# Kernel tuning notes

Hardware: AMD Instinct MI355X
Metric: run time of the kernel (lower is better)

Reference implementation:

```python
import jax, jax.numpy as jnp
import numpy as np

B, DIM, OC, H, W, HEADS = 4, 128, 128, 128, 128, 8
L = H * W
_BN_INV = 1.0 / (1.0 + 1e-5) ** 0.5  # eval-mode BN: running_mean=0, running_var=1


def conv2d(x, w, b=None, groups=1, pad=0):
    y = jax.lax.conv_general_dilated(
        x, w, (1, 1), [(pad, pad), (pad, pad)],
        dimension_numbers=('NCHW', 'OIHW', 'NCHW'),
        feature_group_count=groups)
    if b is not None:
        y = y + b[None, :, None, None]
    return y


def bn(x, g, b):
    return x * (g * _BN_INV)[None, :, None, None] + b[None, :, None, None]


def ln(x, g, b, eps=1e-5):
    m = jnp.mean(x, -1, keepdims=True)
    v = jnp.mean((x - m) ** 2, -1, keepdims=True)
    return (x - m) * jax.lax.rsqrt(v + eps) * g + b


def rope_tables(h, w, c, base=10000.0):
    k_max = c // 4
    theta = 1.0 / base ** (np.arange(k_max, dtype=np.float32) / k_max)
    gi, gj = np.meshgrid(np.arange(h, dtype=np.float32),
                         np.arange(w, dtype=np.float32), indexing='ij')
    ang = np.concatenate([gi[..., None] * theta, gj[..., None] * theta], -1)  # (h,w,c//2)
    return jnp.asarray(np.cos(ang)), jnp.asarray(np.sin(ang))


def apply_rope(x, cs, sn):  # x: (b,h,w,c); consecutive pairs = (re, im)
    xr, xi = x[..., 0::2], x[..., 1::2]
    return jnp.stack([cs * xr - sn * xi, sn * xr + cs * xi], -1).reshape(x.shape)


def linear_attn(x, qk_w, qk_b, lepe_w, lepe_b, h, w):
    b, n, c = x.shape
    hd = c // HEADS
    qk = x @ qk_w.T + qk_b
    q = jax.nn.elu(qk[..., :c]) + 1.0
    k = jax.nn.elu(qk[..., c:]) + 1.0
    cs, sn = rope_tables(h, w, c)

    def heads(t):  # (b,n,c) -> (b,HEADS,n,hd)
        return t.reshape(b, n, HEADS, hd).transpose(0, 2, 1, 3)

    q_r = heads(apply_rope(q.reshape(b, h, w, c), cs, sn).reshape(b, n, c))
    k_r = heads(apply_rope(k.reshape(b, h, w, c), cs, sn).reshape(b, n, c))
    qh, kh, vh = heads(q), heads(k), heads(x)
    k_mean = jnp.mean(kh, axis=2, keepdims=True)                      # (b,Hd,1,hd)
    z = 1.0 / (jnp.einsum('bhnd,bhmd->bhnm', qh, k_mean) + 1e-6)      # (b,Hd,n,1)
    s = n ** -0.5
    kv = jnp.einsum('bhnd,bhne->bhde', k_r * s, vh * s)               # (b,Hd,hd,hd)
    out = jnp.einsum('bhnd,bhde->bhne', q_r, kv) * z
    out = out.transpose(0, 2, 1, 3).reshape(b, n, c)
    v_img = x.reshape(b, h, w, c).transpose(0, 3, 1, 2)
    lepe = conv2d(v_img, lepe_w, lepe_b, groups=c, pad=1)
    return out + lepe.transpose(0, 2, 3, 1).reshape(b, n, c)


def fmt_block(xb, fw1, fb1, f_g, f_be, fw2, fb2, n_g, n_be):
    t = jnp.fft.fft2(xb)                                              # (B,C,H,W) complex
    wgt = jax.nn.relu(bn(conv2d(t.real, fw1, fb1), f_g, f_be))
    wgt = jax.nn.sigmoid(conv2d(wgt, fw2, fb2))
    f = jnp.abs(jnp.fft.ifft2(wgt * t))
    f = jax.nn.relu(bn(f, n_g, n_be))
    return f.reshape(f.shape[0], f.shape[1], -1).transpose(0, 2, 1)   # (B,L,C)


def _forward(x, c1_w, c1_b, c1_g, c1_be, cpe1_w, cpe1_b,
             fw1, fb1, f_g, f_be, fw2, fb2, nbn_g, nbn_be,
             ln1_g, ln1_b, d3w1, d3b1, d3w2, d5w1, d5b1, d5w2,
             ap_w, ap_b, ip2_w, ip2_b, dwc2_w, dwc2_b,
             qk_w, qk_b, lepe_w, lepe_b, op_w, op_b,
             cpe2_w, cpe2_b, ln2_g, ln2_b,
             ffn_w1, ffn_b1, ffn_w2, ffn_b2, po_w,
             red_w, red_b, red_g, red_be):
    Bb, C, Hh, Ww = x.shape
    Ll = Hh * Ww
    to_img = lambda t: t.reshape(Bb, Hh, Ww, C).transpose(0, 3, 1, 2)   # (B,L,C)->(B,C,H,W)
    to_seq = lambda t: t.transpose(0, 2, 3, 1).reshape(Bb, Ll, -1)       # (B,C,H,W)->(B,L,C)

    x_0 = jax.nn.relu(bn(conv2d(x, c1_w, c1_b), c1_g, c1_be))           # (B,OC,H,W)
    xt = to_seq(x + conv2d(x, cpe1_w, cpe1_b, groups=C, pad=1))
    shortcut = xt
    fmt1 = fmt_block(to_img(xt), fw1, fb1, f_g, f_be, fw2, fb2, nbn_g, nbn_be)

    x_s = ln(xt, ln1_g, ln1_b)
    xs_img = to_img(x_s)
    x_s3 = conv2d(conv2d(xs_img, d3w1, d3b1), d3w2, None, groups=C // 2, pad=1)
    x_s5 = conv2d(conv2d(xs_img, d5w1, d5b1), d5w2, None, groups=C // 2, pad=2)
    act_res = jax.nn.silu(to_seq(conv2d(xs_img, ap_w, ap_b)))

    def branch(t):  # (B,C/2,H,W) -> (B,L,C/2)
        t = conv2d(t, ip2_w, ip2_b)
        t = jax.nn.silu(conv2d(t, dwc2_w, dwc2_b, groups=C // 2, pad=1))
        return to_seq(t)

    a3 = linear_attn(branch(x_s3), qk_w, qk_b, lepe_w, lepe_b, Hh, Ww)
    a5 = linear_attn(branch(x_s5), qk_w, qk_b, lepe_w, lepe_b, Hh, Ww)
    xs = jnp.concatenate([a3, a5], -1)
    xs = to_seq(conv2d(to_img(xs * act_res), op_w, op_b))

    xt = shortcut + xs + fmt1
    xt = xt + to_seq(conv2d(to_img(xt), cpe2_w, cpe2_b, groups=C, pad=1))
    fmt2 = fmt_block(to_img(xt), fw1, fb1, f_g, f_be, fw2, fb2, nbn_g, nbn_be)
    h2 = ln(xt, ln2_g, ln2_b)
    ffn = jax.nn.gelu(h2 @ ffn_w1.T + ffn_b1, approximate=False) @ ffn_w2.T + ffn_b2
    xt = xt + ffn + fmt2

    xo = conv2d(to_img(xt), po_w)                                        # (B,OC,H,W)
    cat = jnp.concatenate([x_0, xo], 1)
    return jax.nn.relu(bn(conv2d(cat, red_w, red_b), red_g, red_be)) + x_0


def setup_inputs():
    key = jax.random.key(0)
    it = iter(jax.random.split(key, 64))

    def w(shape, s=0.05):
        return jax.random.normal(next(it), shape, jnp.float32) * s

    d, oc = DIM, OC
    ones = lambda n: jnp.ones((n,), jnp.float32)
    zeros = lambda n: jnp.zeros((n,), jnp.float32)
    return {
        'x': jax.random.normal(next(it), (B, d, H, W), jnp.float32),
        'c1_w': w((oc, d, 1, 1)), 'c1_b': w((oc,), 0.01), 'c1_g': ones(oc), 'c1_be': zeros(oc),
        'cpe1_w': w((d, 1, 3, 3)), 'cpe1_b': w((d,), 0.01),
        'fw1': w((d // 16, d, 1, 1)), 'fb1': w((d // 16,), 0.01),
        'f_g': ones(d // 16), 'f_be': zeros(d // 16),
        'fw2': w((d, d // 16, 1, 1)), 'fb2': w((d,), 0.01),
        'nbn_g': ones(d), 'nbn_be': zeros(d),
        'ln1_g': ones(d), 'ln1_b': zeros(d),
        'd3w1': w((d, d, 1, 1)), 'd3b1': w((d,), 0.01), 'd3w2': w((d // 2, 2, 3, 3)),
        'd5w1': w((d, d, 1, 1)), 'd5b1': w((d,), 0.01), 'd5w2': w((d // 2, 2, 5, 5)),
        'ap_w': w((d, d, 1, 1)), 'ap_b': w((d,), 0.01),
        'ip2_w': w((d // 2, d // 2, 1, 1)), 'ip2_b': w((d // 2,), 0.01),
        'dwc2_w': w((d // 2, 1, 3, 3)), 'dwc2_b': w((d // 2,), 0.01),
        'qk_w': w((d, d // 2)), 'qk_b': w((d,), 0.01),
        'lepe_w': w((d // 2, 1, 3, 3)), 'lepe_b': w((d // 2,), 0.01),
        'op_w': w((d, d, 1, 1)), 'op_b': w((d,), 0.01),
        'cpe2_w': w((d, 1, 3, 3)), 'cpe2_b': w((d,), 0.01),
        'ln2_g': ones(d), 'ln2_b': zeros(d),
        'ffn_w1': w((4, d)), 'ffn_b1': w((4,), 0.01),
        'ffn_w2': w((d, 4)), 'ffn_b2': w((d,), 0.01),
        'po_w': w((oc, d, 1, 1)),
        'red_w': w((oc, 2 * oc, 1, 1)), 'red_b': w((oc,), 0.01),
        'red_g': ones(oc), 'red_be': zeros(oc),
    }


def reference(x, c1_w, c1_b, c1_g, c1_be, cpe1_w, cpe1_b,
              fw1, fb1, f_g, f_be, fw2, fb2, nbn_g, nbn_be,
              ln1_g, ln1_b, d3w1, d3b1, d3w2, d5w1, d5b1, d5w2,
              ap_w, ap_b, ip2_w, ip2_b, dwc2_w, dwc2_b,
              qk_w, qk_b, lepe_w, lepe_b, op_w, op_b,
              cpe2_w, cpe2_b, ln2_g, ln2_b,
              ffn_w1, ffn_b1, ffn_w2, ffn_b2, po_w,
              red_w, red_b, red_g, red_be):
    return _forward(x, c1_w, c1_b, c1_g, c1_be, cpe1_w, cpe1_b,
                    fw1, fb1, f_g, f_be, fw2, fb2, nbn_g, nbn_be,
                    ln1_g, ln1_b, d3w1, d3b1, d3w2, d5w1, d5b1, d5w2,
                    ap_w, ap_b, ip2_w, ip2_b, dwc2_w, dwc2_b,
                    qk_w, qk_b, lepe_w, lepe_b, op_w, op_b,
                    cpe2_w, cpe2_b, ln2_g, ln2_b,
                    ffn_w1, ffn_b1, ffn_w2, ffn_b2, po_w,
                    red_w, red_b, red_g, red_be)
```

## Files before the change

kernel.cpp:

```cpp
#include <hip/hip_runtime.h>
#include <math.h>

typedef unsigned short bf16_t;
typedef __attribute__((ext_vector_type(8))) short short8;
typedef __attribute__((ext_vector_type(4))) float f32x4;

#define B_ 4
#define C_ 128
#define H_ 128
#define W_ 128
#define L_ (H_*W_)
#define NS  ((size_t)B_*L_*C_)
#define NH  ((size_t)B_*L_*64)
#define NSP ((size_t)L_*C_)
#define PI_F 3.14159265358979323846f
#define BN_INV 0.9999950000374997f
#define THETA_SC 0.8304820237218406f
#define TOTW 157148
#define W16SHIFT 107548
#define WOFF_PO 107612
#define WOFF_RED 123996

#define W2_ 66
#define L2_ (128*W2_)
// ... 230 lines not shown
  }
}

__global__ __launch_bounds__(256) void k_fft_col_inv_scaled_h(
    bf16_t* __restrict__ re, bf16_t* __restrict__ im,
    const float* __restrict__ wg1, const float* __restrict__ fw2,
    const float* __restrict__ fb2) {
  __shared__ float Lre[128][34];
  __shared__ float Lim[128][34];
  __shared__ float w2r[8];
  int tid = threadIdx.x;
  size_t img = blockIdx.x >> 1;
  int c = (int)(img & 127);
  int b = (int)(img >> 7);
  int w0 = (blockIdx.x & 1) * 33;
  if (tid < 8) w2r[tid] = fw2[c*8 + tid];
  float b2 = fb2[c];
  bf16_t* rp = re + img * (size_t)L2_ + w0;
  bf16_t* ip = im + img * (size_t)L2_ + w0;
  const float* wgp = wg1 + (size_t)b*8*L2_ + w0;
  __syncthreads();
  for (int i = tid; i < 4224; i += 256) {
    int h = i / 33, wl = i - h*33;
    size_t p = (size_t)h*W2_ + wl;
    float a = b2;
    #pragma unroll
    for (int o = 0; o < 8; o++) a += w2r[o] * wgp[(size_t)o*L2_ + p];
    float wgt = 1.f/(1.f+expf(-a));
    Lre[h][wl] = ldf(rp[p]) * wgt;
    Lim[h][wl] = ldf(ip[p]) * wgt;
  }
  __syncthreads();
  int lane = tid & 63, wv = tid >> 6;
  float tc[7], ts[7];
  tw_inv(lane, tc, ts);
  for (int col = wv; col < 33; col += 4) {
    float lor = Lre[lane][col], loi = Lim[lane][col];
    float hir = Lre[lane+64][col], hii = Lim[lane+64][col];
    fft128_inv(lor, loi, hir, hii, lane, tc, ts);
    Lre[lane][col]=lor*(1.f/128.f); Lim[lane][col]=loi*(1.f/128.f);
    Lre[lane+64][col]=hir*(1.f/128.f); Lim[lane+64][col]=hii*(1.f/128.f);
  }
  __syncthreads();
  for (int i = tid; i < 4224; i += 256) {
    int h = i / 33, wl = i - h*33;
    rp[(size_t)h*W2_ + wl] = f2b(Lre[h][wl]);
    ip[(size_t)h*W2_ + wl] = f2b(Lim[h][wl]);
  }
}

__global__ __launch_bounds__(256) void k_fft_row_inv_abs_seq_h(
    const bf16_t* __restrict__ re, const bf16_t* __restrict__ im,
    const float* __restrict__ ng, const float* __restrict__ nbe,
    const float* __restrict__ add1, const float* __restrict__ add2,
    float* __restrict__ out) {
  __shared__ float S[64*132];
  int tid = threadIdx.x;
  int bid = blockIdx.x;
  int ch = (bid & 1) * 64;
  int h  = (bid >> 1) & 127;
  int b  = bid >> 8;
  {
    const bf16_t* rbase = re + (size_t)(b*128 + ch)*L2_ + (size_t)h*W2_;
    const bf16_t* ibase = im + (size_t)(b*128 + ch)*L2_ + (size_t)h*W2_;
    for (int i = tid; i < 64*66; i += 256) {
      int c = i / 66, v = i - c*66;
      S[c*132 + v]      = ldf(rbase[(size_t)c*L2_ + v]);
      S[c*132 + 66 + v] = ldf(ibase[(size_t)c*L2_ + v]);
    }
  }
  __syncthreads();
  int lane = tid & 63, wv = tid >> 6;
  int rb = (int)(__brev((unsigned)lane) >> 26);
  int vlo = 2*rb, vhi = vlo + 1;
  float tc[7], ts[7];
  tw_inv(lane, tc, ts);
  float rr[8][4];
  #pragma unroll
  for (int t = 0; t < 8; t++) {
    int ca = wv*16 + 2*t, cb = ca + 1;
    const float* Sa = S + ca*132;
    const float* Sb = S + cb*132;
    float lor, loi, hir, hii;
    if (vlo <= 64) {
      float ar = Sa[vlo], ai = Sa[66+vlo], br = Sb[vlo], bi = Sb[66+vlo];
      lor = ar - bi; loi = ai + br;
    } else {
      int u = 128 - vlo;
      float ar = Sa[u], ai = Sa[66+u], br = Sb[u], bi = Sb[66+u];
      lor = ar + bi; loi = br - ai;
    }
    if (vhi <= 64) {
      float ar = Sa[vhi], ai = Sa[66+vhi], br = Sb[vhi], bi = Sb[66+vhi];
      hir = ar - bi; hii = ai + br;
    } else {
      int u = 128 - vhi;
      float ar = Sa[u], ai = Sa[66+u], br = Sb[u], bi = Sb[66+u];
      hir = ar + bi; hii = br - ai;
    }
    fft128_inv(lor, loi, hir, hii, lane, tc, ts);
    rr[t][0] = fabsf(lor);
    rr[t][1] = fabsf(loi);
    rr[t][2] = fabsf(hir);
    rr[t][3] = fabsf(hii);
  }
  __syncthreads();
  float* T = S;
  #pragma unroll
  for (int t = 0; t < 8; t++) {
    int ca = wv*16 + 2*t, cb = ca + 1;
    float sga = ng[ch+ca]*BN_INV, sba = nbe[ch+ca];
    float sgb = ng[ch+cb]*BN_INV, sbb = nbe[ch+cb];
    T[ca*130 + lane]      = fmaxf(rr[t][0]*(1.f/128.f)*sga + sba, 0.f);
    T[cb*130 + lane]      = fmaxf(rr[t][1]*(1.f/128.f)*sgb + sbb, 0.f);
    T[ca*130 + 64 + lane] = fmaxf(rr[t][2]*(1.f/128.f)*sga + sba, 0.f);
    T[cb*130 + 64 + lane] = fmaxf(rr[t][3]*(1.f/128.f)*sgb + sbb, 0.f);
  }
  __syncthreads();
  size_t sb0 = ((size_t)b*L_ + (size_t)h*128)*128 + ch;
  #pragma unroll
  for (int it = 0; it < 8; it++) {
    int idx = it*256 + tid;
    int c4 = (idx & 15)*4, w = idx >> 4;
    size_t off = sb0 + (size_t)w*128 + c4;
    float4 v;
    v.x = T[(c4+0)*130 + w];
    v.y = T[(c4+1)*130 + w];
    v.z = T[(c4+2)*130 + w];
    v.w = T[(c4+3)*130 + w];
    float4 x1 = *(const float4*)(add1 + off);
    float4 x2 = *(const float4*)(add2 + off);
    v.x += x1.x + x2.x; v.y += x1.y + x2.y;
    v.z += x1.z + x2.z; v.w += x1.w + x2.w;
    *(float4*)(out + off) = v;
  }
}

__global__ __launch_bounds__(256) void k_freq1_h(const bf16_t* __restrict__ tre,
    const float* __restrict__ fw1, const float* __restrict__ fb1,
    const float* __restrict__ fg, const float* __restrict__ fbe,
    float* __restrict__ wg1) {
  __shared__ float w1s[1024];
  int tid = threadIdx.x;
  for (int i = tid; i < 1024; i += 256) w1s[i] = fw1[i];
  __syncthreads();
  size_t g = (size_t)blockIdx.x*256 + tid;
  int p = (int)(g % L2_);
  int b = (int)(g / L2_);
  const bf16_t* tp = tre + (size_t)b*128*L2_ + p;
  float acc[8];
  #pragma unroll
  for (int o = 0; o < 8; o++) acc[o] = 0.f;
  for (int c = 0; c < 128; c++) {
    float v = ldf(tp[(size_t)c*L2_]);
    #pragma unroll
    for (int o = 0; o < 8; o++) acc[o] += w1s[o*128+c]*v;
  }
  size_t ob = (size_t)b*8*L2_ + p;
  #pragma unroll
  for (int o = 0; o < 8; o++) {
    float v = (acc[o] + fb1[o]) * (fg[o]*BN_INV) + fbe[o];
    wg1[ob + (size_t)o*L2_] = fmaxf(v, 0.f);
  }
}

template<bool DUAL>
__global__ void k_p2s(const void* __restrict__ src, float* __restrict__ dst,
                      const float* __restrict__ add1, const float* __restrict__ add2,
                      const int* __restrict__ flagp) {
  __shared__ float tile[32][33];
  int fl = DUAL ? *flagp : 1;
  int b = blockIdx.z;
  int p0 = blockIdx.x*32, c0 = blockIdx.y*32;
  int tx = threadIdx.x, ty = threadIdx.y;
  size_t base_in = (size_t)b*NSP;
  #pragma unroll
  for (int k = 0; k < 4; k++) {
    size_t off = base_in + (size_t)(c0+ty+8*k)*L_ + p0 + tx;
    float v;
    if (DUAL && !fl) v = ldf(((const bf16_t*)src)[off]);
    else             v = ((const float*)src)[off];
    tile[ty+8*k][tx] = v;
  }
  __syncthreads();
  size_t base = (size_t)b*NSP;
  #pragma unroll
  for (int k = 0; k < 4; k++) {
    size_t idx = base + (size_t)(p0+ty+8*k)*C_ + c0 + tx;
    float v = tile[tx][ty+8*k];
    if (add1) v += add1[idx];
    if (add2) v += add2[idx];
    dst[idx] = v;
  }
}

template<int CC>
__global__ __launch_bounds__(256) void k_dw3(const float* __restrict__ in,
    const float* __restrict__ w, const float* __restrict__ bias,
    float* __restrict__ out) {
  __shared__ float wl[9*CC];
  int tid = threadIdx.x;
  for (int i = tid; i < 9*CC; i += 256) {
    int tap = i / CC, ch = i % CC;
    wl[i] = w[ch*9 + tap];
  }
  __syncthreads();
  size_t g = (size_t)blockIdx.x*256 + tid;
  int c = (int)(g & (CC-1));
  float wr[9];
  #pragma unroll
  for (int t = 0; t < 9; t++) wr[t] = wl[t*CC + c];
  size_t s = g / CC;
  int w0 = (int)(s & 31) * 4;
  int hp = (int)((s >> 5) & 127);
  int b  = (int)(s >> 12);
  const float* ip = in + (size_t)b*L_*CC + c;
  float bi = bias[c];
  float a0 = bi, a1 = bi, a2 = bi, a3 = bi;
  #pragma unroll
  for (int dh = -1; dh <= 1; dh++) {
    int h2 = hp + dh;
    if ((unsigned)h2 >= 128u) continue;
    const float* rp = ip + (size_t)h2*W_*CC;
    float px[6];
    #pragma unroll
    for (int x = 0; x < 6; x++) {
      int w2 = w0 - 1 + x;
      px[x] = ((unsigned)w2 < 128u) ? rp[(size_t)w2*CC] : 0.f;
    }
    #pragma unroll
    for (int dw = 0; dw < 3; dw++) {
      float f = wr[(dh+1)*3 + dw];
      a0 += f*px[dw];   a1 += f*px[dw+1];
      a2 += f*px[dw+2]; a3 += f*px[dw+3];
    }
  }
  size_t tb = (size_t)b*L_ + (size_t)hp*W_ + w0;
  out[(tb+0)*CC + c] = in[(tb+0)*CC + c] + a0;
  out[(tb+1)*CC + c] = in[(tb+1)*CC + c] + a1;
  out[(tb+2)*CC + c] = in[(tb+2)*CC + c] + a2;
  out[(tb+3)*CC + c] = in[(tb+3)*CC + c] + a3;
}

__global__ __launch_bounds__(256) void k_dw3h(const bf16_t* __restrict__ in,
    const float* __restrict__ w, const float* __restrict__ bias,
    bf16_t* __restrict__ out) {
  __shared__ float wl[9*64];
  int tid = threadIdx.x;
  for (int i = tid; i < 9*64; i += 256) {
    int tap = i / 64, ch = i % 64;
    wl[i] = w[ch*9 + tap];
  }
  __syncthreads();
  size_t g = (size_t)blockIdx.x*256 + tid;
  int c = (int)(g & 63);
  float wr[9];
  #pragma unroll
  for (int t = 0; t < 9; t++) wr[t] = wl[t*64 + c];
  size_t s = g >> 6;
  int w0 = (int)(s & 31) * 4;
  int hp = (int)((s >> 5) & 127);
  int b  = (int)(s >> 12);
  const bf16_t* ip = in + (size_t)b*L_*64 + c;
  float bi = bias[c];
  float a0 = bi, a1 = bi, a2 = bi, a3 = bi;
  #pragma unroll
  for (int dh = -1; dh <= 1; dh++) {
    int h2 = hp + dh;
    if ((unsigned)h2 >= 128u) continue;
    const bf16_t* rp = ip + (size_t)h2*W_*64;
    float px[6];
    #pragma unroll
    for (int x = 0; x < 6; x++) {
      int w2 = w0 - 1 + x;
      px[x] = ((unsigned)w2 < 128u) ? ldf(rp[(size_t)w2*64]) : 0.f;
    }
    #pragma unroll
    for (int dw = 0; dw < 3; dw++) {
      float f = wr[(dh+1)*3 + dw];
      a0 += f*px[dw];   a1 += f*px[dw+1];
      a2 += f*px[dw+2]; a3 += f*px[dw+3];
    }
  }
  size_t tb = (size_t)b*L_ + (size_t)hp*W_ + w0;
  out[(tb+0)*64 + c] = f2b(a0 / (1.f + expf(-a0)));
  out[(tb+1)*64 + c] = f2b(a1 / (1.f + expf(-a1)));
  out[(tb+2)*64 + c] = f2b(a2 / (1.f + expf(-a2)));
  out[(tb+3)*64 + c] = f2b(a3 / (1.f + expf(-a3)));
}

template<int K>
__global__ __launch_bounds__(256) void k_gconv(const bf16_t* __restrict__ in,
    const float* __restrict__ w, bf16_t* __restrict__ out) {
  __shared__ float wl[K*K*128];
// ... 16 lines not shown
  int hp = (int)((s >> 5) & 127);
  int b  = (int)(s >> 12);
  const bf16_t* ip = in + (size_t)b*L_*128 + 2*oc;
  constexpr int P = K/2;
  float a0 = 0.f, a1 = 0.f, a2 = 0.f, a3 = 0.f;
  #pragma unroll
  for (int kh = 0; kh < K; kh++) {
    int h2 = hp + kh - P;
    if ((unsigned)h2 >= 128u) continue;
    const bf16_t* rp = ip + (size_t)h2*W_*128;
    float2 px[K+3];
    #pragma unroll
    for (int x = 0; x < K+3; x++) {
      int w2 = w0 - P + x;
      if ((unsigned)w2 < 128u) {
        unsigned uv = *(const unsigned*)(rp + (size_t)w2*128);
        px[x] = make_float2(ldf((bf16_t)(uv & 0xffffu)), ldf((bf16_t)(uv >> 16)));
      } else px[x] = make_float2(0.f, 0.f);
    }
    #pragma unroll
    for (int kw = 0; kw < K; kw++) {
      float fx = wx[kh*K + kw], fy = wy[kh*K + kw];
      a0 += fx*px[kw+0].x + fy*px[kw+0].y;
      a1 += fx*px[kw+1].x + fy*px[kw+1].y;
      a2 += fx*px[kw+2].x + fy*px[kw+2].y;
      a3 += fx*px[kw+3].x + fy*px[kw+3].y;
    }
  }
  size_t tb = (size_t)b*L_ + (size_t)hp*W_ + w0;
  out[(tb+0)*64 + oc] = f2b(a0);
  out[(tb+1)*64 + oc] = f2b(a1);
  out[(tb+2)*64 + oc] = f2b(a2);
  out[(tb+3)*64 + oc] = f2b(a3);
}

template<int CIN, int COUT, int EPI, bool MUL, bool IB16, bool OB16>
__global__ __launch_bounds__(256) void k_mfma_tok(
    const void* __restrict__ in, const bf16_t* __restrict__ mulp,
    const bf16_t* __restrict__ W16, const float* __restrict__ bias,
    void* __restrict__ out) {
  constexpr int NO = COUT/16;
  constexpr int KS = (CIN >= 128) ? 4 : (CIN/32);
  int tid = threadIdx.x;
  int lane = tid & 63, wv = tid >> 6;
  int m = lane & 15, q = lane >> 4;
  size_t t0 = (size_t)blockIdx.x*64 + (size_t)wv*16;
  f32x4 acc[NO];
  #pragma unroll
  for (int i = 0; i < NO; i++) acc[i] = (f32x4){0.f,0.f,0.f,0.f};
  for (int kc = 0; kc < CIN; kc += KS*32) {
    short8 afv[KS];
    if (IB16) {
      #pragma unroll
      for (int kk = 0; kk < KS; kk++)
        afv[kk] = *(const short8*)((const bf16_t*)in + (t0 + m)*CIN + kc + kk*32 + q*8);
    } else {
      float4 A[KS][2];
      #pragma unroll
      for (int kk = 0; kk < KS; kk++) {
        const float* ap = (const float*)in + (t0 + m)*CIN + kc + kk*32 + q*8;
        A[kk][0] = *(const float4*)ap;
        A[kk][1] = *(const float4*)(ap + 4);
      }
      if (MUL) {
        #pragma unroll
        for (int kk = 0; kk < KS; kk++) {
          const bf16_t* mp = mulp + (t0 + m)*CIN + kc + kk*32 + q*8;
          union { bf16_t u[8]; short8 v; } mv;
          mv.v = *(const short8*)mp;
          A[kk][0].x*=ldf(mv.u[0]); A[kk][0].y*=ldf(mv.u[1]);
          A[kk][0].z*=ldf(mv.u[2]); A[kk][0].w*=ldf(mv.u[3]);
          A[kk][1].x*=ldf(mv.u[4]); A[kk][1].y*=ldf(mv.u[5]);
          A[kk][1].z*=ldf(mv.u[6]); A[kk][1].w*=ldf(mv.u[7]);
        }
      }
      #pragma unroll
      for (int kk = 0; kk < KS; kk++) {
        union { short s[8]; short8 v; } af;
        af.s[0]=(short)f2b(A[kk][0].x); af.s[1]=(short)f2b(A[kk][0].y);
        af.s[2]=(short)f2b(A[kk][0].z); af.s[3]=(short)f2b(A[kk][0].w);
        af.s[4]=(short)f2b(A[kk][1].x); af.s[5]=(short)f2b(A[kk][1].y);
        af.s[6]=(short)f2b(A[kk][1].z); af.s[7]=(short)f2b(A[kk][1].w);
        afv[kk] = af.v;
      }
    }
    #pragma unroll
    for (int kk = 0; kk < KS; kk++) {
      #pragma unroll
      for (int o = 0; o < NO; o++) {
        short8 bf = *(const short8*)(W16 + (size_t)(o*16 + m)*CIN + kc + kk*32 + q*8);
        acc[o] = __builtin_amdgcn_mfma_f32_16x16x32_bf16(afv[kk], bf, acc[o], 0, 0, 0);
      }
    }
  }
  #pragma unroll
  for (int o = 0; o < NO; o++) {
    float bv = (EPI >= 1) ? bias[o*16 + m] : 0.f;
    #pragma unroll
    for (int r = 0; r < 4; r++) {
      int row = q*4 + r;
      float v = acc[o][r] + bv;
      if (EPI == 2) v = v / (1.f + expf(-v));
      if (EPI == 3) v = v > 0.f ? v + 1.f : expf(v);
      size_t idx = (t0 + row)*COUT + o*16 + m;
      if (OB16) ((bf16_t*)out)[idx] = f2b(v);
      else      ((float*)out)[idx] = v;
    }
  }
}

__global__ __launch_bounds__(256) void k_mfma_ln3(
    const float* __restrict__ in,
    const float* __restrict__ lng, const float* __restrict__ lnb,
    const bf16_t* __restrict__ Wd3, const float* __restrict__ bd3,
    const bf16_t* __restrict__ Wd5, const float* __restrict__ bd5,
    const bf16_t* __restrict__ Wap, const float* __restrict__ bap,
    bf16_t* __restrict__ outd3, bf16_t* __restrict__ outd5, bf16_t* __restrict__ outap) {
  __shared__ float gs[128], bs[128];
  __shared__ bf16_t T16[64*130];
  int tid = threadIdx.x;
  if (tid < 128) { gs[tid] = lng[tid]; bs[tid] = lnb[tid]; }
  __syncthreads();
  int lane = tid & 63, wv = tid >> 6;
  int m = lane & 15, q = lane >> 4;
  size_t t0 = (size_t)blockIdx.x*64 + (size_t)wv*16;
  size_t t0blk = (size_t)blockIdx.x*64;
  float4 A[4][2];
// ... 25 lines not shown
      const float* vp = (const float*)&A[kk][h];
      #pragma unroll
      for (int j = 0; j < 4; j++) {
        int c = kk*32 + q*8 + h*4 + j;
        float x = (vp[j] - mean)*inv*gs[c] + bs[c];
        u.sh[h*4+j] = (short)f2b(x);
      }
    }
    af[kk] = u.v;
  }
  f32x4 acc[24];
  #pragma unroll
  for (int i = 0; i < 24; i++) acc[i] = (f32x4){0.f,0.f,0.f,0.f};
  #pragma unroll
  for (int kk = 0; kk < 4; kk++) {
    #pragma unroll
    for (int o = 0; o < 8; o++) {
      size_t woff = (size_t)(o*16 + m)*128 + kk*32 + q*8;
      short8 b3 = *(const short8*)(Wd3 + woff);
      acc[o]    = __builtin_amdgcn_mfma_f32_16x16x32_bf16(af[kk], b3, acc[o],    0, 0, 0);
      short8 b5 = *(const short8*)(Wd5 + woff);
      acc[8+o]  = __builtin_amdgcn_mfma_f32_16x16x32_bf16(af[kk], b5, acc[8+o],  0, 0, 0);
      short8 ba = *(const short8*)(Wap + woff);
      acc[16+o] = __builtin_amdgcn_mfma_f32_16x16x32_bf16(af[kk], ba, acc[16+o], 0, 0, 0);
    }
  }
  #pragma unroll
  for (int mi = 0; mi < 3; mi++) {
    const float* bp = (mi == 0) ? bd3 : (mi == 1) ? bd5 : bap;
    bf16_t* op = (mi == 0) ? outd3 : (mi == 1) ? outd5 : outap;
    #pragma unroll
    for (int o = 0; o < 8; o++) {
      float bv = bp[o*16 + m];
      #pragma unroll
      for (int r = 0; r < 4; r++) {
        float v = acc[mi*8 + o][r] + bv;
        if (mi == 2) v = v / (1.f + expf(-v));
        T16[(wv*16 + q*4 + r)*130 + o*16 + m] = f2b(v);
      }
    }
    __syncthreads();
    for (int i = tid; i < 1024; i += 256) {
      int tok = i >> 4, c0 = (i & 15) * 8;
      union { bf16_t u[8]; short8 v; } pk;
      #pragma unroll
      for (int j = 0; j < 8; j++) pk.u[j] = T16[tok*130 + c0 + j];
      *(short8*)(op + (t0blk + tok)*128 + c0) = pk.v;
    }
    __syncthreads();
  }
}

__global__ __launch_bounds__(256) void k_mfma_c1(
    const float* __restrict__ in, const bf16_t* __restrict__ W16,
    const float* __restrict__ bias, const float* __restrict__ gam,
    const float* __restrict__ bet, bf16_t* __restrict__ out) {
  __shared__ bf16_t T16[64*130];
  constexpr int NO = 8;
  int tid = threadIdx.x;
  int lane = tid & 63, wv = tid >> 6;
  int m = lane & 15, q = lane >> 4;
  size_t t0 = (size_t)blockIdx.x*64 + (size_t)wv*16;
  size_t t0blk = (size_t)blockIdx.x*64;
  f32x4 acc[NO];
  #pragma unroll
  for (int i = 0; i < NO; i++) acc[i] = (f32x4){0.f,0.f,0.f,0.f};
  {
    float4 A[4][2];
    #pragma unroll
    for (int kk = 0; kk < 4; kk++) {
      const float* ap = in + (t0 + m)*128 + kk*32 + q*8;
      A[kk][0] = *(const float4*)ap;
      A[kk][1] = *(const float4*)(ap + 4);
    }
    #pragma unroll
    for (int kk = 0; kk < 4; kk++) {
      union { short s[8]; short8 v; } af;
      af.s[0]=(short)f2b(A[kk][0].x); af.s[1]=(short)f2b(A[kk][0].y);
      af.s[2]=(short)f2b(A[kk][0].z); af.s[3]=(short)f2b(A[kk][0].w);
      af.s[4]=(short)f2b(A[kk][1].x); af.s[5]=(short)f2b(A[kk][1].y);
      af.s[6]=(short)f2b(A[kk][1].z); af.s[7]=(short)f2b(A[kk][1].w);
      #pragma unroll
      for (int o = 0; o < NO; o++) {
        short8 bf = *(const short8*)(W16 + (size_t)(o*16 + m)*128 + kk*32 + q*8);
        acc[o] = __builtin_amdgcn_mfma_f32_16x16x32_bf16(af.v, bf, acc[o], 0, 0, 0);
      }
    }
  }
  #pragma unroll
  for (int o = 0; o < NO; o++) {
    int oc = o*16 + m;
    float bi = bias[oc], gm = gam[oc]*BN_INV, be = bet[oc];
    #pragma unroll
    for (int r = 0; r < 4; r++) {
      float v = acc[o][r] + bi;
      T16[(wv*16 + q*4 + r)*130 + oc] = f2b(fmaxf(v*gm + be, 0.f));
    }
  }
  __syncthreads();
  for (int i = tid; i < 1024; i += 256) {
    int tok = i >> 4, c0 = (i & 15) * 8;
    union { bf16_t u[8]; short8 v; } pk;
    #pragma unroll
    for (int j = 0; j < 8; j++) pk.u[j] = T16[tok*130 + c0 + j];
    *(short8*)(out + (t0blk + tok)*128 + c0) = pk.v;
  }
}

__global__ __launch_bounds__(256) void k_mfma_red(
    const bf16_t* __restrict__ x0s, const float* __restrict__ xt4,
    const bf16_t* __restrict__ W16, const float* __restrict__ bias,
    const float* __restrict__ gam, const float* __restrict__ bet,
    void* __restrict__ out, const int* __restrict__ flagp) {
  __shared__ float T[128*65];
  constexpr int NO = 8;
  int fl = *flagp;
  int tid = threadIdx.x;
  int lane = tid & 63, wv = tid >> 6;
  int m = lane & 15, q = lane >> 4;
  size_t t0 = (size_t)blockIdx.x*64;
  size_t tw = t0 + (size_t)wv*16;
  f32x4 acc[NO];
  #pragma unroll
  for (int i = 0; i < NO; i++) acc[i] = (f32x4){0.f,0.f,0.f,0.f};
  #pragma unroll
  for (int kk = 0; kk < 4; kk++) {
    short8 afv = *(const short8*)(x0s + (tw + m)*128 + kk*32 + q*8);
    #pragma unroll
    for (int o = 0; o < NO; o++) {
      short8 bf = *(const short8*)(W16 + (size_t)(o*16 + m)*256 + kk*32 + q*8);
      acc[o] = __builtin_amdgcn_mfma_f32_16x16x32_bf16(afv, bf, acc[o], 0, 0, 0);
    }
  }
  {
    float4 A[4][2];
    #pragma unroll
    for (int kk = 0; kk < 4; kk++) {
      const float* ap = xt4 + (tw + m)*128 + kk*32 + q*8;
      A[kk][0] = *(const float4*)ap;
      A[kk][1] = *(const float4*)(ap + 4);
    }
    #pragma unroll
    for (int kk = 0; kk < 4; kk++) {
      union { short s[8]; short8 v; } af;
      af.s[0]=(short)f2b(A[kk][0].x); af.s[1]=(short)f2b(A[kk][0].y);
      af.s[2]=(short)f2b(A[kk][0].z); af.s[3]=(short)f2b(A[kk][0].w);
      af.s[4]=(short)f2b(A[kk][1].x); af.s[5]=(short)f2b(A[kk][1].y);
      af.s[6]=(short)f2b(A[kk][1].z); af.s[7]=(short)f2b(A[kk][1].w);
      #pragma unroll
      for (int o = 0; o < NO; o++) {
        short8 bf = *(const short8*)(W16 + (size_t)(o*16 + m)*256 + 128 + kk*32 + q*8);
        acc[o] = __builtin_amdgcn_mfma_f32_16x16x32_bf16(af.v, bf, acc[o], 0, 0, 0);
      }
    }
  }
  #pragma unroll
  for (int ot = 0; ot < NO; ot++) {
    int o = ot*16 + m;
    float bi = bias[o], gm = gam[o]*BN_INV, be = bet[o];
    #pragma unroll
    for (int r = 0; r < 4; r++) {
      int row = q*4 + r;
      float v = acc[ot][r] + bi;
      v = fmaxf(v*gm + be, 0.f);
      v += ldf(x0s[(tw + row)*128 + o]);
      T[o*65 + wv*16 + row] = v;
    }
  }
  __syncthreads();
  int b = (int)(t0 >> 14);
  int p0 = (int)(t0 & (L_-1));
  if (!fl) {
    bf16_t* op = (bf16_t*)out;
    for (int i = tid; i < 8192; i += 256) {
      int o = i >> 6, tk = i & 63;
      op[((size_t)b*128 + o)*L_ + p0 + tk] = f2b(T[o*65 + tk]);
    }
  } else {
    float* op = (float*)out;
    for (int i = tid; i < 8192; i += 256) {
      int o = i >> 6, tk = i & 63;
      op[((size_t)b*128 + o)*L_ + p0 + tk] = T[o*65 + tk];
    }
  }
}

__global__ __launch_bounds__(256) void k_ln_ffn(const float* __restrict__ in,
    const float* __restrict__ g, const float* __restrict__ be,
    const float* __restrict__ w1, const float* __restrict__ b1,
    const float* __restrict__ w2, const float* __restrict__ b2,
    float* __restrict__ out) {
  int tid = threadIdx.x, lane = tid & 63;
  size_t t = (size_t)blockIdx.x*4 + (tid >> 6);
  const float* row = in + t*128;
  float2 v = *(const float2*)(row + lane*2);
  float s = v.x + v.y, ss = v.x*v.x + v.y*v.y;
  #pragma unroll
  for (int m = 1; m < 64; m <<= 1) { s += __shfl_xor(s, m); ss += __shfl_xor(ss, m); }
  float mean = s*(1.f/128.f);
  float inv = rsqrtf(ss*(1.f/128.f) - mean*mean + 1e-5f);
  float hx = (v.x-mean)*inv*g[lane*2]   + be[lane*2];
  float hy = (v.y-mean)*inv*g[lane*2+1] + be[lane*2+1];
  float hp0 = hx*w1[0*128+lane*2] + hy*w1[0*128+lane*2+1];
  float hp1 = hx*w1[1*128+lane*2] + hy*w1[1*128+lane*2+1];
  float hp2 = hx*w1[2*128+lane*2] + hy*w1[2*128+lane*2+1];
  float hp3 = hx*w1[3*128+lane*2] + hy*w1[3*128+lane*2+1];
  #pragma unroll
  for (int m = 1; m < 64; m <<= 1) {
    hp0 += __shfl_xor(hp0, m); hp1 += __shfl_xor(hp1, m);
    hp2 += __shfl_xor(hp2, m); hp3 += __shfl_xor(hp3, m);
  }
  float hv0, hv1, hv2, hv3;
  { float a = hp0 + b1[0]; hv0 = 0.5f*a*(1.f+erff(a*0.7071067811865476f)); }
  { float a = hp1 + b1[1]; hv1 = 0.5f*a*(1.f+erff(a*0.7071067811865476f)); }
  { float a = hp2 + b1[2]; hv2 = 0.5f*a*(1.f+erff(a*0.7071067811865476f)); }
  { float a = hp3 + b1[3]; hv3 = 0.5f*a*(1.f+erff(a*0.7071067811865476f)); }
  int cx = lane*2, cy = lane*2+1;
  float2 o;
  o.x = hv0*w2[cx*4+0] + hv1*w2[cx*4+1] + hv2*w2[cx*4+2] + hv3*w2[cx*4+3] + b2[cx];
  o.y = hv0*w2[cy*4+0] + hv1*w2[cy*4+1] + hv2*w2[cy*4+2] + hv3*w2[cy*4+3] + b2[cy];
  *(float2*)(out + t*128 + lane*2) = o;
}

__global__ __launch_bounds__(256) void k_kv(
    const bf16_t* __restrict__ qk, const bf16_t* __restrict__ v,
    float* __restrict__ akv_g, float* __restrict__ aks_g) {
  __shared__ float kvred[512];
  __shared__ float ksred[64];
  int tid = threadIdx.x;
  for (int i = tid; i < 512; i += 256) kvred[i] = 0.f;
  if (tid < 64) ksred[tid] = 0.f;
  __syncthreads();
  int lane = tid & 63, wv = tid >> 6;
  size_t t0 = (size_t)blockIdx.x * 64;
  int b = (int)(t0 >> 14);
  int pr = lane >> 1;
  float theta = exp2f(-(float)(pr & 15) * THETA_SC);
  bool use_i = pr < 16;
  int hbase = lane & 56;
  float akv[8];
  #pragma unroll
  for (int d = 0; d < 8; d++) akv[d] = 0.f;
  float aks = 0.f;
  for (int it = 0; it < 16; it++) {
    size_t t = t0 + (size_t)wv*16 + it;
    float k = ldf(qk[t*128 + 64 + lane]);
    float xv = ldf(v[t*64 + lane]);
    int l = (int)(t & (L_-1));
    float pos = use_i ? (float)(l >> 7) : (float)(l & 127);
    float sn, cs; sincosf(pos*theta, &sn, &cs);
    float kp = __shfl_xor(k, 1);
    float kr = (lane & 1) ? (sn*kp + cs*k) : (cs*k - sn*kp);
    #pragma unroll
    for (int d = 0; d < 8; d++) {
      float krd = __shfl(kr, hbase + d);
      akv[d] += krd * xv;
    }
    aks += k;
  }
  int h8 = lane >> 3, e = lane & 7;
  #pragma unroll
  for (int d = 0; d < 8; d++)
    atomicAdd(&kvred[h8*64 + d*8 + e], akv[d]);
  atomicAdd(&ksred[lane], aks);
  __syncthreads();
  for (int i = tid; i < 512; i += 256) atomicAdd(&akv_g[b*512 + i], kvred[i]);
  if (tid < 64) atomicAdd(&aks_g[b*64 + tid], ksred[tid]);
}

__global__ __launch_bounds__(256) void k_attn2(
    const bf16_t* __restrict__ qk, const bf16_t* __restrict__ x,
    const float* __restrict__ akv_g, const float* __restrict__ aks_g,
    const float* __restrict__ lw, const float* __restrict__ lb,
    float* __restrict__ out, int coff) {
  __shared__ float kv[512];
  __shared__ float km[64];
  __shared__ float lwl[576];
  int tid = threadIdx.x;
  size_t t0 = (size_t)blockIdx.x * 32;
  int b = (int)(t0 >> 14);
  const float invn = 1.f/16384.f;
  for (int i = tid; i < 512; i += 256) kv[i] = akv_g[b*512 + i]*invn;
  if (tid < 64) km[tid] = aks_g[b*64 + tid]*invn;
  for (int i = tid; i < 576; i += 256) lwl[i] = lw[i];
  __syncthreads();
  int lane = tid & 63, wv = tid >> 6;
  int pr = lane >> 1;
  float theta = exp2f(-(float)(pr & 15) * THETA_SC);
  bool use_i = pr < 16;
  int hbase = lane & 56, e = lane & 7;
  float lbv = lb[lane];
  const bf16_t* xb = x + ((size_t)b << 14) * 64;
  for (int it = 0; it < 8; it++) {
    size_t t = t0 + (size_t)wv*8 + it;
    int l = (int)(t & (L_-1));
    int ipos = l >> 7, jpos = l & 127;
    float q = ldf(qk[t*128 + lane]);
    float p = q * km[lane];
    p += __shfl_xor(p, 1); p += __shfl_xor(p, 2); p += __shfl_xor(p, 4);
    float z = 1.f/(p + 1e-6f);
    float pos = use_i ? (float)ipos : (float)jpos;
    float sn, cs; sincosf(pos*theta, &sn, &cs);
    float qp = __shfl_xor(q, 1);
    float qr = (lane & 1) ? (sn*qp + cs*q) : (cs*q - sn*qp);
    float acc = 0.f;
    #pragma unroll
    for (int d = 0; d < 8; d++) {
      float qrd = __shfl(qr, hbase + d);
      acc += qrd * kv[hbase*8 + d*8 + e];
    }
    acc *= z;
    float lp = lbv;
    #pragma unroll
    for (int dh = -1; dh <= 1; dh++) {
      int h2 = ipos + dh; if ((unsigned)h2 >= 128u) continue;
      #pragma unroll
      for (int dw = -1; dw <= 1; dw++) {
        int w2 = jpos + dw; if ((unsigned)w2 >= 128u) continue;
        lp += lwl[lane*9 + (dh+1)*3 + (dw+1)] * ldf(xb[((size_t)(h2 << 7) + w2)*64 + lane]);
      }
    }
    out[t*128 + coff + lane] = acc + lp;
  }
}

extern "C" void kernel_launch(void* const* d_in, const int* in_sizes, int n_in,
                              void* d_out, int out_size, void* d_ws, size_t ws_size,
                              hipStream_t stream) {
  (void)in_sizes; (void)n_in; (void)out_size;

  float* base;
  if (ws_size >= WSF * sizeof(float)) {
    base = (float*)d_ws;
  } else {
    void* p = nullptr;
    hipGetSymbolAddress(&p, HIP_SYMBOL(g_ws));
    base = (float*)p;
  }
  float* P0 = base;
  float* PA = base + 1*NS;
  float* PB = base + 2*NS;
  float* PC = base + 3*NS;
  float* PD = base + 4*NS;
  float* PF = base + 5*NS;
  float* H0 = base + 6*NS;
  float* H1 = H0 + NH;
  float* H2 = H1 + NH;
  float* WG = H2 + NH;
  float* ACC = WG + WGSLOT;
  float* CW  = ACC + ACCSZ;
  bf16_t* CW16 = (bf16_t*)(CW + CWSZ);
  int*   FLG = (int*)(CW + CWSZ + CW16SZF);

  static const int wsz[47] = {
    16384,128,128,128,1152,128,1024,8,8,8,1024,128,128,128,128,128,
    16384,128,1152,16384,128,3200,16384,128,4096,64,576,64,8192,128,
    576,64,16384,128,1152,128,128,128,512,4,512,128,16384,32768,128,128,128};
  int woff[47]; { int a = 0; for (int i = 0; i < 47; i++){ woff[i] = a; a += wsz[i]; } }
  const float* Wf[47]; for (int i = 0; i < 47; i++) Wf[i] = CW + woff[i];
  auto W16 = [&](int i){ return (const bf16_t*)(CW16 + woff[i] + (woff[i] >= W16SHIFT ? 4 : 0)); };
  const float *c1_b=Wf[1], *c1_g=Wf[2], *c1_be=Wf[3], *cpe1_w=Wf[4],
    *cpe1_b=Wf[5], *fw1=Wf[6], *fb1=Wf[7], *f_g=Wf[8], *f_be=Wf[9], *fw2=Wf[10],
    *fb2=Wf[11], *nbn_g=Wf[12], *nbn_be=Wf[13], *ln1_g=Wf[14], *ln1_b=Wf[15],
    *d3b1=Wf[17], *d3w2=Wf[18], *d5b1=Wf[20],
    *d5w2=Wf[21], *ap_b=Wf[23], *ip2_b=Wf[25],
    *dwc2_w=Wf[26], *dwc2_b=Wf[27], *qk_b=Wf[29], *lepe_w=Wf[30],
    *lepe_b=Wf[31], *op_b=Wf[33], *cpe2_w=Wf[34], *cpe2_b=Wf[35],
    *ln2_g=Wf[36], *ln2_b=Wf[37], *ffn_w1=Wf[38], *ffn_b1=Wf[39], *ffn_w2=Wf[40],
    *ffn_b2=Wf[41], *red_b=Wf[44], *red_g=Wf[45], *red_be=Wf[46];
  const bf16_t *c1_w16=W16(0), *d3w1_16=W16(16), *d5w1_16=W16(19), *ap_w16=W16(22),
    *ip2_w16=W16(24), *qk_w16=W16(28), *op_w16=W16(32), *red_w16=W16(43);

  const void* x = d_in[0];

  k_probe<<<1, 256, 0, stream>>>((const bf16_t*)x, FLG);
  P47 ps; for (int i = 0; i < 47; i++) ps.p[i] = d_in[i+1];
  k_cvt<<<(TOTW+255)/256, 256, 0, stream>>>(ps, FLG, CW);
  k_cvt16<<<(TOTW+255)/256, 256, 0, stream>>>(CW, CW16);
  k_fuse_red<<<64, 256, 0, stream>>>(CW + WOFF_PO, CW + WOFF_RED,
                                     (bf16_t*)(CW16 + WOFF_RED + 4));

  dim3 tgrid(512, 4, 4), tblk(32, 8);

  auto fmt_fused = [&](const float* seq_in, bf16_t* re, bf16_t* im,
                       const float* add1, const float* add2, float* outp) {
    k_fft_row_fwd_half<<<1024, 256, 0, stream>>>(seq_in, re, im);
    k_fft_col_fwd_h<<<1024, 256, 0, stream>>>(re, im);
    k_freq1_h<<<132, 256, 0, stream>>>(re, fw1, fb1, f_g, f_be, WG);
    k_fft_col_inv_scaled_h<<<1024, 256, 0, stream>>>(re, im, WG, fw2, fb2);
    k_fft_row_inv_abs_seq_h<<<1024, 256, 0, stream>>>(re, im, nbn_g, nbn_be, add1, add2, outp);
  };

  auto attn = [&](const bf16_t* brin, float* qkbuf, int coff) {
    k_zero<<<9, 256, 0, stream>>>(ACC, 2304);
    k_mfma_tok<64,128,3,false,true,true><<<1024, 256, 0, stream>>>(brin, nullptr, qk_w16, qk_b, qkbuf);
    k_kv<<<1024, 256, 0, stream>>>((const bf16_t*)qkbuf, brin, ACC, ACC + B_*512);
    k_attn2<<<2048, 256, 0, stream>>>((const bf16_t*)qkbuf, brin, ACC, ACC + B_*512, lepe_w, lepe_b, PF, coff);
  };

  k_p2s<true><<<tgrid, tblk, 0, stream>>>(x, PA, nullptr, nullptr, FLG);
  k_mfma_c1<<<1024, 256, 0, stream>>>(PA, c1_w16, c1_b, c1_g, c1_be, (bf16_t*)P0);
  k_dw3<128><<<8192, 256, 0, stream>>>(PA, cpe1_w, cpe1_b, PB);
  k_mfma_ln3<<<1024, 256, 0, stream>>>(PB, ln1_g, ln1_b,
      d3w1_16, d3b1, d5w1_16, d5b1, ap_w16, ap_b,
      (bf16_t*)PD, (bf16_t*)PF, (bf16_t*)PA);
  k_gconv<3><<<4096, 256, 0, stream>>>((const bf16_t*)PD, d3w2, (bf16_t*)H0);
  k_gconv<5><<<4096, 256, 0, stream>>>((const bf16_t*)PF, d5w2, (bf16_t*)H1);
  k_mfma_tok<64,64,1,false,true,true><<<1024, 256, 0, stream>>>((const bf16_t*)H0, nullptr, ip2_w16, ip2_b, (bf16_t*)H2);
  k_dw3h<<<4096, 256, 0, stream>>>((const bf16_t*)H2, dwc2_w, dwc2_b, (bf16_t*)H0);
  attn((const bf16_t*)H0, PD, 0);
  k_mfma_tok<64,64,1,false,true,true><<<1024, 256, 0, stream>>>((const bf16_t*)H1, nullptr, ip2_w16, ip2_b, (bf16_t*)H2);
  k_dw3h<<<4096, 256, 0, stream>>>((const bf16_t*)H2, dwc2_w, dwc2_b, (bf16_t*)H1);
  attn((const bf16_t*)H1, PD, 64);
  k_mfma_tok<128,128,1,true,false,false><<<1024, 256, 0, stream>>>(PF, (const bf16_t*)PA, op_w16, op_b, PF);
  fmt_fused(PB, (bf16_t*)PC, (bf16_t*)PD, PB, PF, PB);
  k_dw3<128><<<8192, 256, 0, stream>>>(PB, cpe2_w, cpe2_b, PC);
  k_ln_ffn<<<16384, 256, 0, stream>>>(PC, ln2_g, ln2_b, ffn_w1, ffn_b1, ffn_w2, ffn_b2, PF);
  fmt_fused(PC, (bf16_t*)PB, (bf16_t*)PD, PC, PF, PC);
  k_mfma_red<<<1024, 256, 0, stream>>>((const bf16_t*)P0, PC, red_w16, red_b, red_g, red_be, d_out, FLG);
}
```

Baseline: 914.1 us.

## Store intermediate activations in bf16 to cut memory traffic across kernels

```diff
diff --git a/kernel.cpp b/kernel.cpp
--- a/kernel.cpp
+++ b/kernel.cpp
@@ -306,7 +306,7 @@
 __global__ __launch_bounds__(256) void k_fft_row_inv_abs_seq_h(
     const bf16_t* __restrict__ re, const bf16_t* __restrict__ im,
     const float* __restrict__ ng, const float* __restrict__ nbe,
-    const float* __restrict__ add1, const float* __restrict__ add2,
+    const float* __restrict__ add1, const bf16_t* __restrict__ add2,
     float* __restrict__ out) {
   __shared__ float S[64*132];
   int tid = threadIdx.x;
@@ -383,9 +383,11 @@
     v.z = T[(c4+2)*130 + w];
     v.w = T[(c4+3)*130 + w];
     float4 x1 = *(const float4*)(add1 + off);
-    float4 x2 = *(const float4*)(add2 + off);
-    v.x += x1.x + x2.x; v.y += x1.y + x2.y;
-    v.z += x1.z + x2.z; v.w += x1.w + x2.w;
+    uint2 q2 = *(const uint2*)(add2 + off);
+    v.x += x1.x + ldf((bf16_t)(q2.x & 0xffffu));
+    v.y += x1.y + ldf((bf16_t)(q2.x >> 16));
+    v.z += x1.z + ldf((bf16_t)(q2.y & 0xffffu));
+    v.w += x1.w + ldf((bf16_t)(q2.y >> 16));
     *(float4*)(out + off) = v;
   }
 }
@@ -419,8 +421,7 @@
 }
 
 template<bool DUAL>
-__global__ void k_p2s(const void* __restrict__ src, float* __restrict__ dst,
-                      const float* __restrict__ add1, const float* __restrict__ add2,
+__global__ void k_p2s(const void* __restrict__ src, bf16_t* __restrict__ dst,
                       const int* __restrict__ flagp) {
   __shared__ float tile[32][33];
   int fl = DUAL ? *flagp : 1;
@@ -441,15 +442,12 @@
   #pragma unroll
   for (int k = 0; k < 4; k++) {
     size_t idx = base + (size_t)(p0+ty+8*k)*C_ + c0 + tx;
-    float v = tile[tx][ty+8*k];
-    if (add1) v += add1[idx];
-    if (add2) v += add2[idx];
-    dst[idx] = v;
-  }
-}
-
-template<int CC>
-__global__ __launch_bounds__(256) void k_dw3(const float* __restrict__ in,
+    dst[idx] = f2b(tile[tx][ty+8*k]);
+  }
+}
+
+template<int CC, bool IN16>
+__global__ __launch_bounds__(256) void k_dw3(const void* __restrict__ in_,
     const float* __restrict__ w, const float* __restrict__ bias,
     float* __restrict__ out) {
   __shared__ float wl[9*CC];
@@ -468,19 +466,22 @@
   int w0 = (int)(s & 31) * 4;
   int hp = (int)((s >> 5) & 127);
   int b  = (int)(s >> 12);
-  const float* ip = in + (size_t)b*L_*CC + c;
+  size_t ibase = (size_t)b*L_*CC + c;
   float bi = bias[c];
   float a0 = bi, a1 = bi, a2 = bi, a3 = bi;
   #pragma unroll
   for (int dh = -1; dh <= 1; dh++) {
     int h2 = hp + dh;
     if ((unsigned)h2 >= 128u) continue;
-    const float* rp = ip + (size_t)h2*W_*CC;
+    size_t rbase = ibase + (size_t)h2*W_*CC;
     float px[6];
     #pragma unroll
     for (int x = 0; x < 6; x++) {
       int w2 = w0 - 1 + x;
-      px[x] = ((unsigned)w2 < 128u) ? rp[(size_t)w2*CC] : 0.f;
+      if ((unsigned)w2 < 128u) {
+        px[x] = IN16 ? ldf(((const bf16_t*)in_)[rbase + (size_t)w2*CC])
+                     : ((const float*)in_)[rbase + (size_t)w2*CC];
+      } else px[x] = 0.f;
     }
     #pragma unroll
     for (int dw = 0; dw < 3; dw++) {
@@ -490,10 +491,14 @@
     }
   }
   size_t tb = (size_t)b*L_ + (size_t)hp*W_ + w0;
-  out[(tb+0)*CC + c] = in[(tb+0)*CC + c] + a0;
-  out[(tb+1)*CC + c] = in[(tb+1)*CC + c] + a1;
-  out[(tb+2)*CC + c] = in[(tb+2)*CC + c] + a2;
-  out[(tb+3)*CC + c] = in[(tb+3)*CC + c] + a3;
+  float r0 = IN16 ? ldf(((const bf16_t*)in_)[(tb+0)*CC + c]) : ((const float*)in_)[(tb+0)*CC + c];
+  float r1 = IN16 ? ldf(((const bf16_t*)in_)[(tb+1)*CC + c]) : ((const float*)in_)[(tb+1)*CC + c];
+  float r2 = IN16 ? ldf(((const bf16_t*)in_)[(tb+2)*CC + c]) : ((const float*)in_)[(tb+2)*CC + c];
+  float r3 = IN16 ? ldf(((const bf16_t*)in_)[(tb+3)*CC + c]) : ((const float*)in_)[(tb+3)*CC + c];
+  out[(tb+0)*CC + c] = r0 + a0;
+  out[(tb+1)*CC + c] = r1 + a1;
+  out[(tb+2)*CC + c] = r2 + a2;
+  out[(tb+3)*CC + c] = r3 + a3;
 }
 
 __global__ __launch_bounds__(256) void k_dw3h(const bf16_t* __restrict__ in,
@@ -616,8 +621,18 @@
     short8 afv[KS];
     if (IB16) {
       #pragma unroll
-      for (int kk = 0; kk < KS; kk++)
-        afv[kk] = *(const short8*)((const bf16_t*)in + (t0 + m)*CIN + kc + kk*32 + q*8);
+      for (int kk = 0; kk < KS; kk++) {
+        short8 a = *(const short8*)((const bf16_t*)in + (t0 + m)*CIN + kc + kk*32 + q*8);
+        if (MUL) {
+          short8 mz = *(const short8*)(mulp + (t0 + m)*CIN + kc + kk*32 + q*8);
+          union { short s[8]; short8 v; } ua, um, ur;
+          ua.v = a; um.v = mz;
+          #pragma unroll
+          for (int j = 0; j < 8; j++)
+            ur.s[j] = (short)f2b(ldf((bf16_t)ua.s[j]) * ldf((bf16_t)um.s[j]));
+          afv[kk] = ur.v;
+        } else afv[kk] = a;
+      }
     } else {
       float4 A[KS][2];
       #pragma unroll
@@ -625,18 +640,6 @@
         const float* ap = (const float*)in + (t0 + m)*CIN + kc + kk*32 + q*8;
         A[kk][0] = *(const float4*)ap;
         A[kk][1] = *(const float4*)(ap + 4);
-      }
-      if (MUL) {
-        #pragma unroll
-        for (int kk = 0; kk < KS; kk++) {
-          const bf16_t* mp = mulp + (t0 + m)*CIN + kc + kk*32 + q*8;
-          union { bf16_t u[8]; short8 v; } mv;
-          mv.v = *(const short8*)mp;
-          A[kk][0].x*=ldf(mv.u[0]); A[kk][0].y*=ldf(mv.u[1]);
-          A[kk][0].z*=ldf(mv.u[2]); A[kk][0].w*=ldf(mv.u[3]);
-          A[kk][1].x*=ldf(mv.u[4]); A[kk][1].y*=ldf(mv.u[5]);
-          A[kk][1].z*=ldf(mv.u[6]); A[kk][1].w*=ldf(mv.u[7]);
-        }
       }
       #pragma unroll
       for (int kk = 0; kk < KS; kk++) {
@@ -768,7 +771,7 @@
 }
 
 __global__ __launch_bounds__(256) void k_mfma_c1(
-    const float* __restrict__ in, const bf16_t* __restrict__ W16,
+    const bf16_t* __restrict__ in, const bf16_t* __restrict__ W16,
     const float* __restrict__ bias, const float* __restrict__ gam,
     const float* __restrict__ bet, bf16_t* __restrict__ out) {
   __shared__ bf16_t T16[64*130];
@@ -781,26 +784,13 @@
   f32x4 acc[NO];
   #pragma unroll
   for (int i = 0; i < NO; i++) acc[i] = (f32x4){0.f,0.f,0.f,0.f};
-  {
-    float4 A[4][2];
-    #pragma unroll
-    for (int kk = 0; kk < 4; kk++) {
-      const float* ap = in + (t0 + m)*128 + kk*32 + q*8;
-      A[kk][0] = *(const float4*)ap;
-      A[kk][1] = *(const float4*)(ap + 4);
-    }
-    #pragma unroll
-    for (int kk = 0; kk < 4; kk++) {
-      union { short s[8]; short8 v; } af;
-      af.s[0]=(short)f2b(A[kk][0].x); af.s[1]=(short)f2b(A[kk][0].y);
-      af.s[2]=(short)f2b(A[kk][0].z); af.s[3]=(short)f2b(A[kk][0].w);
-      af.s[4]=(short)f2b(A[kk][1].x); af.s[5]=(short)f2b(A[kk][1].y);
-      af.s[6]=(short)f2b(A[kk][1].z); af.s[7]=(short)f2b(A[kk][1].w);
-      #pragma unroll
-      for (int o = 0; o < NO; o++) {
-        short8 bf = *(const short8*)(W16 + (size_t)(o*16 + m)*128 + kk*32 + q*8);
-        acc[o] = __builtin_amdgcn_mfma_f32_16x16x32_bf16(af.v, bf, acc[o], 0, 0, 0);
-      }
+  #pragma unroll
+  for (int kk = 0; kk < 4; kk++) {
+    short8 afv = *(const short8*)(in + (t0 + m)*128 + kk*32 + q*8);
+    #pragma unroll
+    for (int o = 0; o < NO; o++) {
+      short8 bf = *(const short8*)(W16 + (size_t)(o*16 + m)*128 + kk*32 + q*8);
+      acc[o] = __builtin_amdgcn_mfma_f32_16x16x32_bf16(afv, bf, acc[o], 0, 0, 0);
     }
   }
   #pragma unroll
@@ -905,7 +895,7 @@
     const float* __restrict__ g, const float* __restrict__ be,
     const float* __restrict__ w1, const float* __restrict__ b1,
     const float* __restrict__ w2, const float* __restrict__ b2,
-    float* __restrict__ out) {
+    bf16_t* __restrict__ out) {
   int tid = threadIdx.x, lane = tid & 63;
   size_t t = (size_t)blockIdx.x*4 + (tid >> 6);
   const float* row = in + t*128;
@@ -932,10 +922,10 @@
   { float a = hp2 + b1[2]; hv2 = 0.5f*a*(1.f+erff(a*0.7071067811865476f)); }
   { float a = hp3 + b1[3]; hv3 = 0.5f*a*(1.f+erff(a*0.7071067811865476f)); }
   int cx = lane*2, cy = lane*2+1;
-  float2 o;
-  o.x = hv0*w2[cx*4+0] + hv1*w2[cx*4+1] + hv2*w2[cx*4+2] + hv3*w2[cx*4+3] + b2[cx];
-  o.y = hv0*w2[cy*4+0] + hv1*w2[cy*4+1] + hv2*w2[cy*4+2] + hv3*w2[cy*4+3] + b2[cy];
-  *(float2*)(out + t*128 + lane*2) = o;
+  float ox = hv0*w2[cx*4+0] + hv1*w2[cx*4+1] + hv2*w2[cx*4+2] + hv3*w2[cx*4+3] + b2[cx];
+  float oy = hv0*w2[cy*4+0] + hv1*w2[cy*4+1] + hv2*w2[cy*4+2] + hv3*w2[cy*4+3] + b2[cy];
+  unsigned pk = (unsigned)f2b(ox) | ((unsigned)f2b(oy) << 16);
+  *(unsigned*)(out + t*128 + lane*2) = pk;
 }
 
 __global__ __launch_bounds__(256) void k_kv(
@@ -988,7 +978,7 @@
     const bf16_t* __restrict__ qk, const bf16_t* __restrict__ x,
     const float* __restrict__ akv_g, const float* __restrict__ aks_g,
     const float* __restrict__ lw, const float* __restrict__ lb,
-    float* __restrict__ out, int coff) {
+    bf16_t* __restrict__ out, int coff) {
   __shared__ float kv[512];
   __shared__ float km[64];
   __shared__ float lwl[576];
@@ -1036,7 +1026,7 @@
         lp += lwl[lane*9 + (dh+1)*3 + (dw+1)] * ldf(xb[((size_t)(h2 << 7) + w2)*64 + lane]);
       }
     }
-    out[t*128 + coff + lane] = acc + lp;
+    out[t*128 + coff + lane] = f2b(acc + lp);
   }
 }
 
@@ -1099,7 +1089,7 @@
   dim3 tgrid(512, 4, 4), tblk(32, 8);
 
   auto fmt_fused = [&](const float* seq_in, bf16_t* re, bf16_t* im,
-                       const float* add1, const float* add2, float* outp) {
+                       const float* add1, const bf16_t* add2, float* outp) {
     k_fft_row_fwd_half<<<1024, 256, 0, stream>>>(seq_in, re, im);
     k_fft_col_fwd_h<<<1024, 256, 0, stream>>>(re, im);
     k_freq1_h<<<132, 256, 0, stream>>>(re, fw1, fb1, f_g, f_be, WG);
@@ -1111,12 +1101,12 @@
     k_zero<<<9, 256, 0, stream>>>(ACC, 2304);
     k_mfma_tok<64,128,3,false,true,true><<<1024, 256, 0, stream>>>(brin, nullptr, qk_w16, qk_b, qkbuf);
     k_kv<<<1024, 256, 0, stream>>>((const bf16_t*)qkbuf, brin, ACC, ACC + B_*512);
-    k_attn2<<<2048, 256, 0, stream>>>((const bf16_t*)qkbuf, brin, ACC, ACC + B_*512, lepe_w, lepe_b, PF, coff);
+    k_attn2<<<2048, 256, 0, stream>>>((const bf16_t*)qkbuf, brin, ACC, ACC + B_*512, lepe_w, lepe_b, (bf16_t*)PF, coff);
   };
 
-  k_p2s<true><<<tgrid, tblk, 0, stream>>>(x, PA, nullptr, nullptr, FLG);
-  k_mfma_c1<<<1024, 256, 0, stream>>>(PA, c1_w16, c1_b, c1_g, c1_be, (bf16_t*)P0);
-  k_dw3<128><<<8192, 256, 0, stream>>>(PA, cpe1_w, cpe1_b, PB);
+  k_p2s<true><<<tgrid, tblk, 0, stream>>>(x, (bf16_t*)PA, FLG);
+  k_mfma_c1<<<1024, 256, 0, stream>>>((const bf16_t*)PA, c1_w16, c1_b, c1_g, c1_be, (bf16_t*)P0);
+  k_dw3<128,true><<<8192, 256, 0, stream>>>(PA, cpe1_w, cpe1_b, PB);
   k_mfma_ln3<<<1024, 256, 0, stream>>>(PB, ln1_g, ln1_b,
       d3w1_16, d3b1, d5w1_16, d5b1, ap_w16, ap_b,
       (bf16_t*)PD, (bf16_t*)PF, (bf16_t*)PA);
@@ -1128,10 +1118,10 @@
   k_mfma_tok<64,64,1,false,true,true><<<1024, 256, 0, stream>>>((const bf16_t*)H1, nullptr, ip2_w16, ip2_b, (bf16_t*)H2);
   k_dw3h<<<4096, 256, 0, stream>>>((const bf16_t*)H2, dwc2_w, dwc2_b, (bf16_t*)H1);
   attn((const bf16_t*)H1, PD, 64);
-  k_mfma_tok<128,128,1,true,false,false><<<1024, 256, 0, stream>>>(PF, (const bf16_t*)PA, op_w16, op_b, PF);
-  fmt_fused(PB, (bf16_t*)PC, (bf16_t*)PD, PB, PF, PB);
-  k_dw3<128><<<8192, 256, 0, stream>>>(PB, cpe2_w, cpe2_b, PC);
-  k_ln_ffn<<<16384, 256, 0, stream>>>(PC, ln2_g, ln2_b, ffn_w1, ffn_b1, ffn_w2, ffn_b2, PF);
-  fmt_fused(PC, (bf16_t*)PB, (bf16_t*)PD, PC, PF, PC);
+  k_mfma_tok<128,128,1,true,true,true><<<1024, 256, 0, stream>>>(PF, (const bf16_t*)PA, op_w16, op_b, PF);
+  fmt_fused(PB, (bf16_t*)PC, (bf16_t*)PD, PB, (const bf16_t*)PF, PB);
+  k_dw3<128,false><<<8192, 256, 0, stream>>>(PB, cpe2_w, cpe2_b, PC);
+  k_ln_ffn<<<16384, 256, 0, stream>>>(PC, ln2_g, ln2_b, ffn_w1, ffn_b1, ffn_w2, ffn_b2, (bf16_t*)PF);
+  fmt_fused(PC, (bf16_t*)PB, (bf16_t*)PD, PC, (const bf16_t*)PF, PC);
   k_mfma_red<<<1024, 256, 0, stream>>>((const bf16_t*)P0, PC, red_w16, red_b, red_g, red_be, d_out, FLG);
 }
```

New measurement: 899.8 us. About the same (-1.6%).
